# Performance work log

Hardware: AMD Instinct MI355X
Metric: run time of the kernel (lower is better)

The kernel has to match this reference:

```python
import jax, jax.numpy as jnp
import numpy as np

B, T1, D, K = 8, 513, 768, 8192  # batch, tokens incl. CLS, feature dim, codebook size


def setup_inputs() -> dict:
    key = jax.random.key(0)
    k1, k2 = jax.random.split(key)
    representation = jax.random.normal(k1, (B, T1, D), dtype=jnp.float32)
    centroids = jax.random.normal(k2, (K, D), dtype=jnp.float32)
    return {"representation": representation, "centroids": centroids}


def reference(representation, centroids):
    # quant_mem_efficient: drop first (CLS) token, L2-distance argmin over codebook
    rep = representation[:, 1:, :]                        # [B, T, D]
    norm_rep = jnp.sum(rep * rep, axis=-1, keepdims=True)  # [B, T, 1]
    norm_cent = jnp.sum(centroids * centroids, axis=-1)    # [K]
    dot = jnp.einsum('btd,kd->btk', rep, centroids)        # [B, T, K]
    distances = norm_rep + norm_cent[None, None, :] - 2.0 * dot
    tokens = jnp.argmin(distances, axis=-1)                # [B, T] int
    # unquant: embedding gather
    quantized = jnp.take(centroids, tokens, axis=0)        # [B, T, D]
    return tokens, quantized
```

## Files before the change

kernel.cpp:

```cpp
#include <hip/hip_runtime.h>
#include <stdint.h>

#define BT 4096
#define KC 8192
#define DD 768
#define T_STRIDE 513
#define DELTA 20.0f

typedef int   v4i  __attribute__((ext_vector_type(4)));
typedef float f32x4 __attribute__((ext_vector_type(4)));

#define GLD16(gp, lp)                                                       \
  __builtin_amdgcn_global_load_lds(                                         \
      (__attribute__((address_space(1))) void*)(gp),                        \
      (__attribute__((address_space(3))) void*)(lp), 16, 0, 0)

__device__ __forceinline__ unsigned int sortable_bits(float d) {
  unsigned int bits = __float_as_uint(d);
  return (bits & 0x80000000u) ? ~bits : (bits | 0x80000000u);
}

__global__ __launch_bounds__(256) void quant_kernel(
    const float* __restrict__ rep, const float* __restrict__ cent,
    int8_t* __restrict__ a8, int8_t* __restrict__ b8,
    float* __restrict__ s_a, float* __restrict__ s_b,
    float* __restrict__ norm_cent) {
  int wid  = (blockIdx.x * blockDim.x + threadIdx.x) >> 6;
  int lane = threadIdx.x & 63;
  const float4* s4;
  int8_t* dst;
  float* sdst;
  float* ndst = nullptr;
  if (wid < BT) {
    int b = wid >> 9, tt = wid & 511;
    s4 = (const float4*)(rep + (size_t)(b * T_STRIDE + 1 + tt) * DD);
    dst = a8 + (size_t)wid * DD;
    sdst = s_a + wid;
  } else {
    int k = wid - BT;
    if (k >= KC) return;
    s4 = (const float4*)(cent + (size_t)k * DD);
    dst = b8 + (size_t)k * DD;
    sdst = s_b + k;
    ndst = norm_cent + k;
  }
  float4 v[3];
  float m = 0.f, nrm = 0.f;
  #pragma unroll
  for (int i = 0; i < 3; ++i) {
    v[i] = s4[lane + i * 64];
    m = fmaxf(m, fmaxf(fmaxf(fabsf(v[i].x), fabsf(v[i].y)),
                       fmaxf(fabsf(v[i].z), fabsf(v[i].w))));
    nrm += v[i].x * v[i].x + v[i].y * v[i].y + v[i].z * v[i].z + v[i].w * v[i].w;
  }
  #pragma unroll
  for (int off = 32; off; off >>= 1) m = fmaxf(m, __shfl_xor(m, off, 64));
  const float rs = (m > 0.f) ? 127.0f / m : 0.f;
  unsigned* d32 = (unsigned*)dst;
  #pragma unroll
  for (int i = 0; i < 3; ++i) {
    int q0 = (int)rintf(v[i].x * rs);
    int q1 = (int)rintf(v[i].y * rs);
    int q2 = (int)rintf(v[i].z * rs);
    int q3 = (int)rintf(v[i].w * rs);
    unsigned pk = (unsigned)(q0 & 255) | ((unsigned)(q1 & 255) << 8) |
                  ((unsigned)(q2 & 255) << 16) | ((unsigned)(q3 & 255) << 24);
    d32[lane + i * 64] = pk;
  }
  if (ndst) {
    #pragma unroll
    for (int off = 32; off; off >>= 1) nrm += __shfl_down(nrm, off, 64);
  }
  if (lane == 0) {
    *sdst = m / 127.0f;
    if (ndst) *ndst = nrm;
  }
}

__global__ __launch_bounds__(512, 1) void mfma_i8_cand(
    const int8_t* __restrict__ a8,
    const int8_t* __restrict__ b8,
    const float* __restrict__ s_a, const float* __restrict__ s_b,
    const float* __restrict__ norm_cent,
    float* __restrict__ LMin, unsigned long long* __restrict__ Mask) {
  __shared__ __attribute__((aligned(16))) int8_t As[3][256 * 64];
  __shared__ __attribute__((aligned(16))) int8_t Bs[3][256 * 64];

  const int tid = threadIdx.x;
  const int w = tid >> 6, l = tid & 63;
  const int bm0 = blockIdx.x * 256;
  const int bn0 = blockIdx.y * 256;

  const int srow   = tid >> 2;
  const int schunk = (tid & 3) ^ (srow & 3);
  const size_t gA0 = (size_t)(bm0 + srow) * DD + schunk * 16;
  const size_t gB0 = (size_t)(bn0 + srow) * DD + schunk * 16;
  const int ls = tid * 16;

  const int wm = (w >> 2) * 128;
  const int wn = (w & 3) * 64;
  const int sub = l & 15, q = l >> 4;
  const int rslot = (q ^ (sub & 3)) * 16;

  v4i acc[8][4] = {};

#define STAGE(kt)                                                             \
  do {                                                                        \
    const int b_ = (kt) % 3;                                                  \
    GLD16(b8 + gA0 + (kt) * 64,            As[b_] + ls);                      \
    GLD16(b8 + gA0 + (size_t)128 * DD + (kt) * 64, As[b_] + 8192 + ls);       \
    GLD16(a8 + gB0 + (kt) * 64,            Bs[b_] + ls);                      \
    GLD16(a8 + gB0 + (size_t)128 * DD + (kt) * 64, Bs[b_] + 8192 + ls);       \
  } while (0)

  STAGE(0);
  STAGE(1);
  asm volatile("s_waitcnt vmcnt(4)" ::: "memory");
  __builtin_amdgcn_s_barrier();
  asm volatile("" ::: "memory");
  __builtin_amdgcn_sched_barrier(0);

  #pragma unroll
  for (int t = 0; t < 12; ++t) {
    const int buf = t % 3;
    v4i af[8], bf[4];
    #pragma unroll
    for (int m = 0; m < 8; ++m)
      af[m] = *(const v4i*)(As[buf] + (wm + m * 16 + sub) * 64 + rslot);
    #pragma unroll
    for (int n = 0; n < 4; ++n)
      bf[n] = *(const v4i*)(Bs[buf] + (wn + n * 16 + sub) * 64 + rslot);
    if (t < 10) STAGE(t + 2);
    __builtin_amdgcn_s_setprio(1);
    #pragma unroll
    for (int m = 0; m < 8; ++m)
      #pragma unroll
      for (int n = 0; n < 4; ++n)
        asm volatile("v_mfma_i32_16x16x64_i8 %0, %1, %2, %0"
                     : "+v"(acc[m][n])
                     : "v"(af[m]), "v"(bf[n]));
    __builtin_amdgcn_s_setprio(0);
    if (t <= 9)       asm volatile("s_waitcnt vmcnt(4)" ::: "memory");
    else if (t == 10) asm volatile("s_waitcnt vmcnt(0)" ::: "memory");
    if (t < 11) {
      __builtin_amdgcn_s_barrier();
      asm volatile("" ::: "memory");
      __builtin_amdgcn_sched_barrier(0);
    }
  }
#undef STAGE

  asm volatile("s_nop 7\n\ts_nop 7\n\ts_nop 7" ::: "memory");

  #pragma unroll
  for (int half = 0; half < 2; ++half) {
    const int g = ((bm0 + wm) >> 6) + half;
    float nc[4][4], sb2[4][4];
    #pragma unroll
    for (int mt = 0; mt < 4; ++mt)
      #pragma unroll
      for (int r = 0; r < 4; ++r) {
        const int k = bm0 + wm + (half * 4 + mt) * 16 + q * 4 + r;
        nc[mt][r] = norm_cent[k];
        sb2[mt][r] = 2.0f * s_b[k];
      }
    #pragma unroll
    for (int nt = 0; nt < 4; ++nt) {
      const int t = bn0 + wn + nt * 16 + sub;
      const float sa = s_a[t];
      float d[4][4];
      float dmin = 3.4e38f;
      #pragma unroll
      for (int mt = 0; mt < 4; ++mt)
        #pragma unroll
        for (int r = 0; r < 4; ++r) {
          d[mt][r] = nc[mt][r] - sa * sb2[mt][r] * (float)acc[half * 4 + mt][nt][r];
          dmin = fminf(dmin, d[mt][r]);
        }
      dmin = fminf(dmin, __shfl_xor(dmin, 16, 64));
      dmin = fminf(dmin, __shfl_xor(dmin, 32, 64));
      const float thresh = dmin + DELTA;
      unsigned long long pm = 0;
      #pragma unroll
      for (int mt = 0; mt < 4; ++mt)
        #pragma unroll
        for (int r = 0; r < 4; ++r)
          if (d[mt][r] <= thresh) pm |= 1ull << (mt * 16 + q * 4 + r);
      pm |= (unsigned long long)__shfl_xor((long long)pm, 16, 64);
      pm |= (unsigned long long)__shfl_xor((long long)pm, 32, 64);
      if (q == 0) {
        LMin[(size_t)t * 128 + g] = dmin;
        Mask[(size_t)t * 128 + g] = pm;
      }
    }
  }
}

__global__ __launch_bounds__(256) void refine_kernel(
    const float* __restrict__ LMin, const unsigned long long* __restrict__ Mask,
    const float* __restrict__ rep, const float* __restrict__ cent,
    const float* __restrict__ norm_cent,
    float* __restrict__ out_tokens, float* __restrict__ out_q) {
  const int w = threadIdx.x >> 6, l = threadIdx.x & 63;
  const int t = blockIdx.x * 4 + w;
  if (t >= BT) return;

  const float lm0 = LMin[(size_t)t * 128 + l];
  const float lm1 = LMin[(size_t)t * 128 + 64 + l];
  float v = fminf(lm0, lm1);
  #pragma unroll
  for (int off = 32; off; off >>= 1) v = fminf(v, __shfl_xor(v, off, 64));
  const float thresh = v + DELTA;
  unsigned long long gm0 = __ballot(lm0 <= thresh);
  unsigned long long gm1 = __ballot(lm1 <= thresh);

  const int b_ = t >> 9, tt = t & 511;
  const float* rrow = rep + (size_t)(b_ * T_STRIDE + 1 + tt) * DD;
  unsigned long long bestE = ~0ull;

  #pragma unroll
  for (int half = 0; half < 2; ++half) {
    unsigned long long gmask = half ? gm1 : gm0;
    while (gmask) {
      const int h = __ffsll((unsigned long long)gmask) - 1;
      gmask &= gmask - 1;
      unsigned long long mask = Mask[(size_t)t * 128 + half * 64 + h];
      while (mask) {
        const int bit = __ffsll((unsigned long long)mask) - 1;
        mask &= mask - 1;
        const int k = (half * 64 + h) * 64 + bit;
        const float* crow = cent + (size_t)k * DD;
        float part = 0.f;
        #pragma unroll
        for (int j = 0; j < 12; ++j)
          part += rrow[l + j * 64] * crow[l + j * 64];
        #pragma unroll
        for (int off = 32; off; off >>= 1) part += __shfl_down(part, off, 64);
        if (l == 0) {
          float d = norm_cent[k] - 2.0f * part;
          unsigned long long p =
              ((unsigned long long)sortable_bits(d) << 32) | (unsigned)k;
          if (p < bestE) bestE = p;
        }
      }
    }
  }
  int kb0 = (l == 0) ? (int)(bestE & 0xFFFFFFFFull) : 0;
  const int kbest = __shfl(kb0, 0, 64);
  if (l == 0) out_tokens[t] = (float)kbest;
  const float4* src = (const float4*)(cent + (size_t)kbest * DD);
  float4* dst = (float4*)(out_q + (size_t)t * DD);
  #pragma unroll
  for (int j = 0; j < 3; ++j) dst[l + j * 64] = src[l + j * 64];
}

#define FBM 64
#define FBN 64
#define FBK 16
#define FNSPLIT 16
__global__ __launch_bounds__(256) void norms_only_kernel(
    const float* __restrict__ rep, const float* __restrict__ cent,
    float* __restrict__ norm_rep, float* __restrict__ norm_cent) {
  int wid  = (blockIdx.x * blockDim.x + threadIdx.x) >> 6;
  int lane = threadIdx.x & 63;
  const float* src;
  float* nd;
  if (wid < BT) {
    int b = wid >> 9, tt = wid & 511;
    src = rep + (size_t)(b * T_STRIDE + 1 + tt) * DD;
    nd = norm_rep + wid;
  } else {
    int k = wid - BT;
    if (k >= KC) return;
    src = cent + (size_t)k * DD;
    nd = norm_cent + k;
  }
  float s = 0.f;
  for (int j = lane; j < DD; j += 64) { float v = src[j]; s += v * v; }
  #pragma unroll
  for (int off = 32; off; off >>= 1) s += __shfl_down(s, off, 64);
  if (lane == 0) *nd = s;
}

__global__ __launch_bounds__(256) void fp32_argmin_gemm(
    const float* __restrict__ rep, const float* __restrict__ cent,
    const float* __restrict__ norm_rep, const float* __restrict__ norm_cent,
    unsigned long long* __restrict__ packed) {
  __shared__ float Asf[FBK][FBM];
  __shared__ float Bsf[FBK][FBN];
  const int tid = threadIdx.x;
  const int m0  = blockIdx.x * FBM;
  const int kbase = blockIdx.y * (KC / FNSPLIT);
  const int tx = tid & 15, ty = tid >> 4;
  const int ldr = tid >> 2, ldc = (tid & 3) * 4;
  const int t_ld = m0 + ldr;
  const float* arow =
      rep + (size_t)((t_ld >> 9) * T_STRIDE + 1 + (t_ld & 511)) * DD + ldc;
  unsigned long long best[4];
  #pragma unroll
  for (int i = 0; i < 4; ++i) best[i] = ~0ull;
  float nr[4];
  #pragma unroll
  for (int i = 0; i < 4; ++i) nr[i] = norm_rep[m0 + ty * 4 + i];
  for (int nt = 0; nt < (KC / FNSPLIT) / FBN; ++nt) {
    const int n0 = kbase + nt * FBN;
    const float* brow = cent + (size_t)(n0 + ldr) * DD + ldc;
    float acc[4][4];
    #pragma unroll
    for (int i = 0; i < 4; ++i)
      #pragma unroll
      for (int j = 0; j < 4; ++j) acc[i][j] = 0.f;
    for (int d0 = 0; d0 < DD; d0 += FBK) {
      float4 av = *(const float4*)(arow + d0);
      float4 bv = *(const float4*)(brow + d0);
      __syncthreads();
      Asf[ldc + 0][ldr] = av.x; Asf[ldc + 1][ldr] = av.y;
      Asf[ldc + 2][ldr] = av.z; Asf[ldc + 3][ldr] = av.w;
      Bsf[ldc + 0][ldr] = bv.x; Bsf[ldc + 1][ldr] = bv.y;
      Bsf[ldc + 2][ldr] = bv.z; Bsf[ldc + 3][ldr] = bv.w;
      __syncthreads();
      #pragma unroll
      for (int kk = 0; kk < FBK; ++kk) {
        float4 a4 = *(const float4*)&Asf[kk][ty * 4];
        float4 b4 = *(const float4*)&Bsf[kk][tx * 4];
        float a[4] = {a4.x, a4.y, a4.z, a4.w};
        float b[4] = {b4.x, b4.y, b4.z, b4.w};
        #pragma unroll
        for (int i = 0; i < 4; ++i)
          #pragma unroll
          for (int j = 0; j < 4; ++j) acc[i][j] += a[i] * b[j];
      }
    }
    #pragma unroll
    for (int i = 0; i < 4; ++i) {
      #pragma unroll
      for (int j = 0; j < 4; ++j) {
        int k = n0 + tx * 4 + j;
        float d = (nr[i] + norm_cent[k]) - 2.0f * acc[i][j];
        unsigned long long p =
            ((unsigned long long)sortable_bits(d) << 32) | (unsigned int)k;
        if (p < best[i]) best[i] = p;
      }
    }
  }
  #pragma unroll
  for (int off = 1; off < 16; off <<= 1) {
    #pragma unroll
    for (int i = 0; i < 4; ++i) {
      unsigned long long o =
          (unsigned long long)__shfl_xor((long long)best[i], off, 64);
      if (o < best[i]) best[i] = o;
    }
  }
  if (tx == 0) {
    #pragma unroll
    for (int i = 0; i < 4; ++i)
      atomicMin(&packed[m0 + ty * 4 + i], best[i]);
  }
}

__global__ __launch_bounds__(192) void gather_kernel(
    const unsigned long long* __restrict__ packed,
    const float* __restrict__ cent,
    float* __restrict__ out_tokens, float* __restrict__ out_q) {
  int t = blockIdx.x;
  unsigned int k = (unsigned int)(packed[t] & 0xFFFFFFFFull);
  if (threadIdx.x == 0) out_tokens[t] = (float)k;
  const float4* src = (const float4*)(cent + (size_t)k * DD);
  float4* dst = (float4*)(out_q + (size_t)t * DD);
  dst[threadIdx.x] = src[threadIdx.x];
}

extern "C" void kernel_launch(void* const* d_in, const int* in_sizes, int n_in,
                              void* d_out, int out_size, void* d_ws, size_t ws_size,
                              hipStream_t stream) {
  const float* rep  = (const float*)d_in[0];
  const float* cent = (const float*)d_in[1];
  float* out = (float*)d_out;

  const size_t SZ_A8 = (size_t)BT * DD;
  const size_t SZ_B8 = (size_t)KC * DD;
  const size_t SZ_LM = (size_t)BT * 128 * 4;
  const size_t SZ_MK = (size_t)BT * 128 * 8;
  const size_t OFF_SA = SZ_A8 + SZ_B8 + SZ_LM + SZ_MK;
  const size_t OFF_SB = OFF_SA + 16384;
  const size_t OFF_NC = OFF_SB + 32768;
  const size_t WS_A   = OFF_NC + 32768;

  if (ws_size >= WS_A) {
    int8_t* a8 = (int8_t*)d_ws;
    int8_t* b8 = (int8_t*)((char*)d_ws + SZ_A8);
    float* LMin = (float*)((char*)d_ws + SZ_A8 + SZ_B8);
    unsigned long long* Mask =
        (unsigned long long*)((char*)d_ws + SZ_A8 + SZ_B8 + SZ_LM);
    float* s_a = (float*)((char*)d_ws + OFF_SA);
    float* s_b = (float*)((char*)d_ws + OFF_SB);
    float* norm_cent = (float*)((char*)d_ws + OFF_NC);

    quant_kernel<<<3072, 256, 0, stream>>>(rep, cent, a8, b8, s_a, s_b,
                                           norm_cent);
    dim3 grid(KC / 256, BT / 256);
    mfma_i8_cand<<<grid, 512, 0, stream>>>(a8, b8, s_a, s_b, norm_cent,
                                           LMin, Mask);
    refine_kernel<<<BT / 4, 256, 0, stream>>>(LMin, Mask, rep, cent,
                                              norm_cent, out, out + BT);
  } else {
    unsigned long long* packed = (unsigned long long*)d_ws;
    float* norm_rep  = (float*)((char*)d_ws + 32768);
    float* norm_cent = (float*)((char*)d_ws + 49152);

    hipMemsetAsync(packed, 0xFF, BT * sizeof(unsigned long long), stream);
    norms_only_kernel<<<3072, 256, 0, stream>>>(rep, cent, norm_rep, norm_cent);
    dim3 grid(BT / FBM, FNSPLIT);
    fp32_argmin_gemm<<<grid, 256, 0, stream>>>(rep, cent, norm_rep, norm_cent,
                                               packed);
    gather_kernel<<<BT, 192, 0, stream>>>(packed, cent, out, out + BT);
  }
}
```

Before: 142.5 us.

## Fuse quantize, int8 MFMA candidate search and refine into one cooperative kernel

Replaces the three-kernel pipeline (quantize, int8 MFMA candidate GEMM, refine/gather) with a single persistent cooperative kernel of 256 blocks that uses grid-wide syncs between phases. Each block quantizes rows in a strided loop, then processes two 256x256 GEMM tiles, then refines two tokens per wave. This removes two kernel launches and their tail gaps, but it limits the GEMM to 256 resident blocks and adds grid-sync costs. The old three-kernel path remains as a fallback if cooperative launch is unsupported or fails.

```diff
diff --git a/kernel.cpp b/kernel.cpp
--- a/kernel.cpp
+++ b/kernel.cpp
@@ -1,5 +1,8 @@
 #include <hip/hip_runtime.h>
+#include <hip/hip_cooperative_groups.h>
 #include <stdint.h>
+
+namespace cg = cooperative_groups;
 
 #define BT 4096
 #define KC 8192
@@ -8,7 +11,6 @@
 #define DELTA 20.0f
 
 typedef int   v4i  __attribute__((ext_vector_type(4)));
-typedef float f32x4 __attribute__((ext_vector_type(4)));
 
 #define GLD16(gp, lp)                                                       \
   __builtin_amdgcn_global_load_lds(                                         \
@@ -18,6 +20,244 @@
 __device__ __forceinline__ unsigned int sortable_bits(float d) {
   unsigned int bits = __float_as_uint(d);
   return (bits & 0x80000000u) ? ~bits : (bits | 0x80000000u);
+}
+
+__global__ __launch_bounds__(512, 1) void fused_vq(
+    const float* __restrict__ rep, const float* __restrict__ cent,
+    int8_t* __restrict__ a8, int8_t* __restrict__ b8,
+    float* __restrict__ s_a, float* __restrict__ s_b,
+    float* __restrict__ norm_cent,
+    float* __restrict__ LMin, unsigned long long* __restrict__ Mask,
+    float* __restrict__ out_tokens, float* __restrict__ out_q) {
+  __shared__ __attribute__((aligned(16))) int8_t As[3][256 * 64];
+  __shared__ __attribute__((aligned(16))) int8_t Bs[3][256 * 64];
+
+  const int tid = threadIdx.x;
+  const int l = tid & 63;
+  const int gw = blockIdx.x * 8 + (tid >> 6);
+
+  #pragma unroll 1
+  for (int i = 0; i < 6; ++i) {
+    const int wid = gw + i * 2048;
+    const float4* s4;
+    int8_t* dq;
+    float* sdst;
+    float* ndst = nullptr;
+    if (wid < BT) {
+      int b = wid >> 9, tt = wid & 511;
+      s4 = (const float4*)(rep + (size_t)(b * T_STRIDE + 1 + tt) * DD);
+      dq = a8 + (size_t)wid * DD;
+      sdst = s_a + wid;
+    } else {
+      int k = wid - BT;
+      s4 = (const float4*)(cent + (size_t)k * DD);
+      dq = b8 + (size_t)k * DD;
+      sdst = s_b + k;
+      ndst = norm_cent + k;
+    }
+    float4 v[3];
+    float m = 0.f, nrm = 0.f;
+    #pragma unroll
+    for (int j = 0; j < 3; ++j) {
+      v[j] = s4[l + j * 64];
+      m = fmaxf(m, fmaxf(fmaxf(fabsf(v[j].x), fabsf(v[j].y)),
+                         fmaxf(fabsf(v[j].z), fabsf(v[j].w))));
+      nrm += v[j].x * v[j].x + v[j].y * v[j].y + v[j].z * v[j].z + v[j].w * v[j].w;
+    }
+    #pragma unroll
+    for (int off = 32; off; off >>= 1) m = fmaxf(m, __shfl_xor(m, off, 64));
+    const float rsc = (m > 0.f) ? 127.0f / m : 0.f;
+    unsigned* d32 = (unsigned*)dq;
+    #pragma unroll
+    for (int j = 0; j < 3; ++j) {
+      int q0 = (int)rintf(v[j].x * rsc);
+      int q1 = (int)rintf(v[j].y * rsc);
+      int q2 = (int)rintf(v[j].z * rsc);
+      int q3 = (int)rintf(v[j].w * rsc);
+      unsigned pk = (unsigned)(q0 & 255) | ((unsigned)(q1 & 255) << 8) |
+                    ((unsigned)(q2 & 255) << 16) | ((unsigned)(q3 & 255) << 24);
+      d32[l + j * 64] = pk;
+    }
+    if (ndst) {
+      #pragma unroll
+      for (int off = 32; off; off >>= 1) nrm += __shfl_down(nrm, off, 64);
+    }
+    if (l == 0) {
+      *sdst = m / 127.0f;
+      if (ndst) *ndst = nrm;
+    }
+  }
+
+  __threadfence();
+  cg::this_grid().sync();
+
+  const int w = tid >> 6;
+  const int srow   = tid >> 2;
+  const int schunk = (tid & 3) ^ (srow & 3);
+  const int ls = tid * 16;
+  const int wm = (w >> 2) * 128;
+  const int wn = (w & 3) * 64;
+  const int sub = l & 15, q = l >> 4;
+  const int rslot = (q ^ (sub & 3)) * 16;
+
+  #pragma unroll 1
+  for (int rp = 0; rp < 2; ++rp) {
+    const int tileId = blockIdx.x + rp * 256;
+    const int bm0 = (tileId & 31) * 256;
+    const int bn0 = (tileId >> 5) * 256;
+    const size_t gA0 = (size_t)(bm0 + srow) * DD + schunk * 16;
+    const size_t gB0 = (size_t)(bn0 + srow) * DD + schunk * 16;
+
+    __syncthreads();
+
+    v4i acc[8][4] = {};
+
+#define STAGE(kt)                                                             \
+  do {                                                                        \
+    const int b_ = (kt) % 3;                                                  \
+    GLD16(b8 + gA0 + (kt) * 64,                    As[b_] + ls);              \
+    GLD16(b8 + gA0 + (size_t)128 * DD + (kt) * 64, As[b_] + 8192 + ls);       \
+    GLD16(a8 + gB0 + (kt) * 64,                    Bs[b_] + ls);              \
+    GLD16(a8 + gB0 + (size_t)128 * DD + (kt) * 64, Bs[b_] + 8192 + ls);       \
+  } while (0)
+
+    STAGE(0);
+    STAGE(1);
+    asm volatile("s_waitcnt vmcnt(4)" ::: "memory");
+    __builtin_amdgcn_s_barrier();
+    asm volatile("" ::: "memory");
+    __builtin_amdgcn_sched_barrier(0);
+
+    #pragma unroll
+    for (int kt = 0; kt < 12; ++kt) {
+      const int buf = kt % 3;
+      v4i af[8], bf[4];
+      #pragma unroll
+      for (int m = 0; m < 8; ++m)
+        af[m] = *(const v4i*)(As[buf] + (wm + m * 16 + sub) * 64 + rslot);
+      #pragma unroll
+      for (int n = 0; n < 4; ++n)
+        bf[n] = *(const v4i*)(Bs[buf] + (wn + n * 16 + sub) * 64 + rslot);
+      if (kt < 10) STAGE(kt + 2);
+      __builtin_amdgcn_s_setprio(1);
+      #pragma unroll
+      for (int m = 0; m < 8; ++m)
+        #pragma unroll
+        for (int n = 0; n < 4; ++n)
+          asm volatile("v_mfma_i32_16x16x64_i8 %0, %1, %2, %0"
+                       : "+v"(acc[m][n])
+                       : "v"(af[m]), "v"(bf[n]));
+      __builtin_amdgcn_s_setprio(0);
+      if (kt <= 9)       asm volatile("s_waitcnt vmcnt(4)" ::: "memory");
+      else if (kt == 10) asm volatile("s_waitcnt vmcnt(0)" ::: "memory");
+      if (kt < 11) {
+        __builtin_amdgcn_s_barrier();
+        asm volatile("" ::: "memory");
+        __builtin_amdgcn_sched_barrier(0);
+      }
+    }
+#undef STAGE
+
+    asm volatile("s_nop 7\n\ts_nop 7\n\ts_nop 7" ::: "memory");
+
+    #pragma unroll
+    for (int half = 0; half < 2; ++half) {
+      const int g = ((bm0 + wm) >> 6) + half;
+      float nc[4][4], sb2[4][4];
+      #pragma unroll
+      for (int mt = 0; mt < 4; ++mt)
+        #pragma unroll
+        for (int r = 0; r < 4; ++r) {
+          const int k = bm0 + wm + (half * 4 + mt) * 16 + q * 4 + r;
+          nc[mt][r] = norm_cent[k];
+          sb2[mt][r] = 2.0f * s_b[k];
+        }
+      #pragma unroll
+      for (int nt = 0; nt < 4; ++nt) {
+        const int t = bn0 + wn + nt * 16 + sub;
+        const float sa = s_a[t];
+        float d[4][4];
+        float dmin = 3.4e38f;
+        #pragma unroll
+        for (int mt = 0; mt < 4; ++mt)
+          #pragma unroll
+          for (int r = 0; r < 4; ++r) {
+            d[mt][r] = nc[mt][r] - sa * sb2[mt][r] * (float)acc[half * 4 + mt][nt][r];
+            dmin = fminf(dmin, d[mt][r]);
+          }
+        dmin = fminf(dmin, __shfl_xor(dmin, 16, 64));
+        dmin = fminf(dmin, __shfl_xor(dmin, 32, 64));
+        const float thresh = dmin + DELTA;
+        unsigned long long pm = 0;
+        #pragma unroll
+        for (int mt = 0; mt < 4; ++mt)
+          #pragma unroll
+          for (int r = 0; r < 4; ++r)
+            if (d[mt][r] <= thresh) pm |= 1ull << (mt * 16 + q * 4 + r);
+        pm |= (unsigned long long)__shfl_xor((long long)pm, 16, 64);
+        pm |= (unsigned long long)__shfl_xor((long long)pm, 32, 64);
+        if (q == 0) {
+          LMin[(size_t)t * 128 + g] = dmin;
+          Mask[(size_t)t * 128 + g] = pm;
+        }
+      }
+    }
+  }
+
+  __threadfence();
+  cg::this_grid().sync();
+
+  #pragma unroll 1
+  for (int i = 0; i < 2; ++i) {
+    const int t = gw + i * 2048;
+    const float lm0 = LMin[(size_t)t * 128 + l];
+    const float lm1 = LMin[(size_t)t * 128 + 64 + l];
+    float v = fminf(lm0, lm1);
+    #pragma unroll
+    for (int off = 32; off; off >>= 1) v = fminf(v, __shfl_xor(v, off, 64));
+    const float thresh = v + DELTA;
+    unsigned long long gm0 = __ballot(lm0 <= thresh);
+    unsigned long long gm1 = __ballot(lm1 <= thresh);
+
+    const int b_ = t >> 9, tt = t & 511;
+    const float* rrow = rep + (size_t)(b_ * T_STRIDE + 1 + tt) * DD;
+    unsigned long long bestE = ~0ull;
+
+    #pragma unroll 1
+    for (int half = 0; half < 2; ++half) {
+      unsigned long long gmask = half ? gm1 : gm0;
+      while (gmask) {
+        const int h = __ffsll((unsigned long long)gmask) - 1;
+        gmask &= gmask - 1;
+        unsigned long long mask = Mask[(size_t)t * 128 + half * 64 + h];
+        while (mask) {
+          const int bit = __ffsll((unsigned long long)mask) - 1;
+          mask &= mask - 1;
+          const int k = (half * 64 + h) * 64 + bit;
+          const float* crow = cent + (size_t)k * DD;
+          float part = 0.f;
+          #pragma unroll
+          for (int j = 0; j < 12; ++j)
+            part += rrow[l + j * 64] * crow[l + j * 64];
+          #pragma unroll
+          for (int off = 32; off; off >>= 1) part += __shfl_down(part, off, 64);
+          if (l == 0) {
+            float d = norm_cent[k] - 2.0f * part;
+            unsigned long long p =
+                ((unsigned long long)sortable_bits(d) << 32) | (unsigned)k;
+            if (p < bestE) bestE = p;
+          }
+        }
+      }
+    }
+    int kb0 = (l == 0) ? (int)(bestE & 0xFFFFFFFFull) : 0;
+    const int kbest = __shfl(kb0, 0, 64);
+    if (l == 0) out_tokens[t] = (float)kbest;
+    const float4* src = (const float4*)(cent + (size_t)kbest * DD);
+    float4* dst = (float4*)(out_q + (size_t)t * DD);
+    #pragma unroll
+    for (int j = 0; j < 3; ++j) dst[l + j * 64] = src[l + j * 64];
+  }
 }
 
 __global__ __launch_bounds__(256) void quant_kernel(
@@ -78,8 +318,7 @@
 }
 
 __global__ __launch_bounds__(512, 1) void mfma_i8_cand(
-    const int8_t* __restrict__ a8,
-    const int8_t* __restrict__ b8,
+    const int8_t* __restrict__ a8, const int8_t* __restrict__ b8,
     const float* __restrict__ s_a, const float* __restrict__ s_b,
     const float* __restrict__ norm_cent,
     float* __restrict__ LMin, unsigned long long* __restrict__ Mask) {
@@ -90,13 +329,11 @@
   const int w = tid >> 6, l = tid & 63;
   const int bm0 = blockIdx.x * 256;
   const int bn0 = blockIdx.y * 256;
-
   const int srow   = tid >> 2;
   const int schunk = (tid & 3) ^ (srow & 3);
   const size_t gA0 = (size_t)(bm0 + srow) * DD + schunk * 16;
   const size_t gB0 = (size_t)(bn0 + srow) * DD + schunk * 16;
   const int ls = tid * 16;
-
   const int wm = (w >> 2) * 128;
   const int wn = (w & 3) * 64;
   const int sub = l & 15, q = l >> 4;
@@ -107,9 +344,9 @@
 #define STAGE(kt)                                                             \
   do {                                                                        \
     const int b_ = (kt) % 3;                                                  \
-    GLD16(b8 + gA0 + (kt) * 64,            As[b_] + ls);                      \
+    GLD16(b8 + gA0 + (kt) * 64,                    As[b_] + ls);              \
     GLD16(b8 + gA0 + (size_t)128 * DD + (kt) * 64, As[b_] + 8192 + ls);       \
-    GLD16(a8 + gB0 + (kt) * 64,            Bs[b_] + ls);                      \
+    GLD16(a8 + gB0 + (kt) * 64,                    Bs[b_] + ls);              \
     GLD16(a8 + gB0 + (size_t)128 * DD + (kt) * 64, Bs[b_] + 8192 + ls);       \
   } while (0)
 
@@ -396,14 +633,36 @@
     float* s_a = (float*)((char*)d_ws + OFF_SA);
     float* s_b = (float*)((char*)d_ws + OFF_SB);
     float* norm_cent = (float*)((char*)d_ws + OFF_NC);
-
-    quant_kernel<<<3072, 256, 0, stream>>>(rep, cent, a8, b8, s_a, s_b,
-                                           norm_cent);
-    dim3 grid(KC / 256, BT / 256);
-    mfma_i8_cand<<<grid, 512, 0, stream>>>(a8, b8, s_a, s_b, norm_cent,
-                                           LMin, Mask);
-    refine_kernel<<<BT / 4, 256, 0, stream>>>(LMin, Mask, rep, cent,
-                                              norm_cent, out, out + BT);
+    float* out_t = out;
+    float* out_q = out + BT;
+
+    static int coop = -1;
+    if (coop < 0) {
+      int dev = 0;
+      (void)hipGetDevice(&dev);
+      if (hipDeviceGetAttribute(&coop, hipDeviceAttributeCooperativeLaunch,
+                                dev) != hipSuccess)
+        coop = 0;
+    }
+
+    bool launched = false;
+    if (coop == 1) {
+      void* kargs[] = {(void*)&rep,  (void*)&cent, (void*)&a8,   (void*)&b8,
+                       (void*)&s_a,  (void*)&s_b,  (void*)&norm_cent,
+                       (void*)&LMin, (void*)&Mask, (void*)&out_t, (void*)&out_q};
+      hipError_t e = hipLaunchCooperativeKernel(
+          (const void*)fused_vq, dim3(256), dim3(512), kargs, 0, stream);
+      launched = (e == hipSuccess);
+    }
+    if (!launched) {
+      quant_kernel<<<3072, 256, 0, stream>>>(rep, cent, a8, b8, s_a, s_b,
+                                             norm_cent);
+      dim3 grid(KC / 256, BT / 256);
+      mfma_i8_cand<<<grid, 512, 0, stream>>>(a8, b8, s_a, s_b, norm_cent,
+                                             LMin, Mask);
+      refine_kernel<<<BT / 4, 256, 0, stream>>>(LMin, Mask, rep, cent,
+                                                norm_cent, out_t, out_q);
+    }
   } else {
     unsigned long long* packed = (unsigned long long*)d_ws;
     float* norm_rep  = (float*)((char*)d_ws + 32768);
```

After: 344.0 us. 2.41x slower.
